# Performance work log

Measured on AMD Instinct MI355X. Metric: run time of the kernel, lower is better.

The kernel has to match this reference:

```python
import jax, jax.numpy as jnp
import numpy as np

BS = 64
DIMS = [1862, 512, 256, 128, 256, 512, 1862]  # layer widths of the generated MLP
W_TOTAL = sum(DIMS[i] * DIMS[i + 1] for i in range(6))   # 2234368
B_TOTAL = sum(DIMS[1:])                                   # 3526


def setup_inputs() -> dict:
    key = jax.random.key(0)
    k1, k2, k3 = jax.random.split(key, 3)
    x = jax.random.normal(k1, (BS, DIMS[0]), dtype=jnp.float32)
    # scale generated weights/biases to keep activations in a sane numeric range
    net_weights = jax.random.normal(k2, (BS, W_TOTAL), dtype=jnp.float32) * 0.02
    net_bias = jax.random.normal(k3, (BS, B_TOTAL), dtype=jnp.float32) * 0.02
    return {"x": x, "net_weights": net_weights, "net_bias": net_bias}


def reference(x, net_weights, net_bias):
    # x: (B, 1862); per-sample weights flattened in net_weights, biases in net_bias.
    h = x
    w_off = 0
    b_off = 0
    for i in range(6):
        din, dout = DIMS[i], DIMS[i + 1]
        W = net_weights[:, w_off:w_off + din * dout].reshape(-1, din, dout)  # (B, din, dout)
        b = net_bias[:, b_off:b_off + dout]                                   # (B, dout)
        h = jnp.einsum('bi,bio->bo', h, W) + b  # batched GEMV + bias
        h = jax.nn.silu(h) if i < 5 else jnp.tanh(h)
        w_off += din * dout
        b_off += dout
    return h[:, None, :]  # (B, 1, 1862), matching torch bmm output shape
```

## Files before the change

kernel.cpp:

```cpp
#include <hip/hip_runtime.h>

#define BS        64
#define W_TOTAL_C 2234368
#define B_TOTAL_C 3526

__device__ __forceinline__ float silu_f(float v) {
    return v / (1.f + __expf(-v));
}

template<int DIN, int DOUT, int KC, int NK, int PNK, int VEC, int BLK,
         bool FINAL, int WOFF, int PBOFF, int FBOFF>
__global__ __launch_bounds__(BLK)
void layer_kernel(const float* __restrict__ hin,
                  const float* __restrict__ wbase,
                  const float* __restrict__ bias,
                  float* __restrict__ outp)
{
    __shared__ float sh[KC];

    const int b   = blockIdx.z;
    const int ky  = blockIdx.y;
    const int k0  = ky * KC;
    const int tid = threadIdx.x;

    for (int i = tid; i < KC; i += BLK) {
        float s;
        if (PNK == 0) {
            s = hin[b * DIN + k0 + i];
        } else {
            s = bias[b * B_TOTAL_C + PBOFF + k0 + i];
            #pragma unroll
            for (int k = 0; k < PNK; ++k)
                s += hin[((size_t)k * BS + b) * DIN + k0 + i];
            s = silu_f(s);
        }
        sh[i] = s;
    }
    __syncthreads();

    const int  o      = (blockIdx.x * BLK + tid) * VEC;
    const bool active = (o < DOUT);

    float a0 = 0.f, a1 = 0.f, a2 = 0.f, a3 = 0.f;
    if (active) {
        const float* wp = wbase + (size_t)b * W_TOTAL_C + WOFF
                                + (size_t)k0 * DOUT + o;
        if (VEC == 4) {
            #pragma unroll 16
            for (int i = 0; i < KC; ++i) {
                const float hv = sh[i];
                const float4 w = *reinterpret_cast<const float4*>(wp);
                a0 = fmaf(hv, w.x, a0);
                a1 = fmaf(hv, w.y, a1);
                a2 = fmaf(hv, w.z, a2);
                a3 = fmaf(hv, w.w, a3);
                wp += DOUT;
            }
        } else {
            #pragma unroll 16
            for (int i = 0; i < KC; ++i) {
                const float hv = sh[i];
                const float2 w = *reinterpret_cast<const float2*>(wp);
                a0 = fmaf(hv, w.x, a0);
                a1 = fmaf(hv, w.y, a1);
                wp += DOUT;
            }
        }
    }

    if (!active) return;

    if (FINAL) {
        float v0 = a0 + bias[b * B_TOTAL_C + FBOFF + o];
        outp[b * DOUT + o] = tanhf(v0);
        if (o + 1 < DOUT) {
            float v1 = a1 + bias[b * B_TOTAL_C + FBOFF + o + 1];
            outp[b * DOUT + o + 1] = tanhf(v1);
        }
    } else {
        float* pp = outp + ((size_t)ky * BS + b) * DOUT + o;
        if (VEC == 4) {
            *reinterpret_cast<float4*>(pp) = make_float4(a0, a1, a2, a3);
        } else {
            pp[0] = a0;
            pp[1] = a1;
        }
    }
}

extern "C" void kernel_launch(void* const* d_in, const int* in_sizes, int n_in,
                              void* d_out, int out_size, void* d_ws, size_t ws_size,
                              hipStream_t stream)
{
    const float* x    = (const float*)d_in[0];
    const float* wts  = (const float*)d_in[1];
    const float* bias = (const float*)d_in[2];
    float* out = (float*)d_out;

    float* p0 = (float*)d_ws;
    float* p1 = p0 + 229376;
    float* p2 = p1 + 65536;
    float* p3 = p2 + 32768;
    float* p4 = p3 + 65536;

    layer_kernel<1862, 512, 266, 7, 0, 4, 128, false,       0,    0,    0>
        <<<dim3(1, 7, BS), 128, 0, stream>>>(x, wts, bias, p0);
    layer_kernel< 512, 256, 128, 4, 7, 2, 128, false,  953344,    0,    0>
        <<<dim3(1, 4, BS), 128, 0, stream>>>(p0, wts, bias, p1);
    layer_kernel< 256, 128,  64, 4, 4, 2,  64, false, 1084416,  512,    0>
        <<<dim3(1, 4, BS),  64, 0, stream>>>(p1, wts, bias, p2);
    layer_kernel< 128, 256,  32, 4, 4, 2, 128, false, 1117184,  768,    0>
        <<<dim3(1, 4, BS), 128, 0, stream>>>(p2, wts, bias, p3);
    layer_kernel< 256, 512,  64, 4, 4, 2, 128, false, 1149952,  896,    0>
        <<<dim3(2, 4, BS), 128, 0, stream>>>(p3, wts, bias, p4);
    layer_kernel< 512, 1862, 512, 1, 4, 2, 256, true, 1281024, 1152, 1664>
        <<<dim3(4, 1, BS), 256, 0, stream>>>(p4, wts, bias, out);
}
```

Baseline: 121.2 us.

## Software-pipeline layers across two batch halves in combined launches

Splits the batch of 64 into two halves of 32 and skews them, so each launch runs layer i for the second half together with layer i+1 for the first half. The goal is to fill the machine in layers that launch too few blocks and to hide launch gaps, at the cost of seven launches instead of six. Layer 0 is also split into 14 K-chunks instead of 7, with a larger partial buffer, and all blocks now use 128 threads. Layer 5 changes from 4 blocks of 256 threads to 8 blocks of 128.

```diff
diff --git a/kernel.cpp b/kernel.cpp
--- a/kernel.cpp
+++ b/kernel.cpp
@@ -1,6 +1,6 @@
 #include <hip/hip_runtime.h>
 
-#define BS        64
+#define BSALL     64
 #define W_TOTAL_C 2234368
 #define B_TOTAL_C 3526
 
@@ -8,85 +8,123 @@
     return v / (1.f + __expf(-v));
 }
 
-template<int DIN, int DOUT, int KC, int NK, int PNK, int VEC, int BLK,
-         bool FINAL, int WOFF, int PBOFF, int FBOFF>
-__global__ __launch_bounds__(BLK)
-void layer_kernel(const float* __restrict__ hin,
-                  const float* __restrict__ wbase,
-                  const float* __restrict__ bias,
-                  float* __restrict__ outp)
+template<int DIN_, int DOUT_, int KC_, int NKY_, int GX_, int PNK_, int VEC_,
+         bool FINAL_, int WOFF_, int PBOFF_, int FBOFF_, int SB_>
+struct LP {
+    static constexpr int  DIN = DIN_, DOUT = DOUT_, KC = KC_, NKY = NKY_,
+                          GX = GX_, PNK = PNK_, VEC = VEC_, WOFF = WOFF_,
+                          PBOFF = PBOFF_, FBOFF = FBOFF_, SB = SB_;
+    static constexpr bool FINAL = FINAL_;
+    static constexpr int  NBLK = GX_ * NKY_ * 32;
+};
+
+template<class P>
+__device__ __forceinline__
+void layer_body(int bid, int tid,
+                const float* __restrict__ hin,
+                float* __restrict__ outp,
+                const float* __restrict__ wbase,
+                const float* __restrict__ bias,
+                float* sh)
 {
-    __shared__ float sh[KC];
+    const int b    = P::SB + (bid & 31);
+    const int rest = bid >> 5;
+    const int ky   = rest % P::NKY;
+    const int gx   = rest / P::NKY;
+    const int k0   = ky * P::KC;
 
-    const int b   = blockIdx.z;
-    const int ky  = blockIdx.y;
-    const int k0  = ky * KC;
-    const int tid = threadIdx.x;
-
-    for (int i = tid; i < KC; i += BLK) {
+    for (int i = tid; i < P::KC; i += 128) {
         float s;
-        if (PNK == 0) {
-            s = hin[b * DIN + k0 + i];
+        if (P::PNK == 0) {
+            s = hin[b * P::DIN + k0 + i];
         } else {
-            s = bias[b * B_TOTAL_C + PBOFF + k0 + i];
+            s = bias[b * B_TOTAL_C + P::PBOFF + k0 + i];
             #pragma unroll
-            for (int k = 0; k < PNK; ++k)
-                s += hin[((size_t)k * BS + b) * DIN + k0 + i];
+            for (int k = 0; k < P::PNK; ++k)
+                s += hin[((size_t)k * BSALL + b) * P::DIN + k0 + i];
             s = silu_f(s);
         }
         sh[i] = s;
     }
     __syncthreads();
 
-    const int  o      = (blockIdx.x * BLK + tid) * VEC;
-    const bool active = (o < DOUT);
+    const int o = (gx * 128 + tid) * P::VEC;
+    if (o >= P::DOUT) return;
 
     float a0 = 0.f, a1 = 0.f, a2 = 0.f, a3 = 0.f;
-    if (active) {
-        const float* wp = wbase + (size_t)b * W_TOTAL_C + WOFF
-                                + (size_t)k0 * DOUT + o;
-        if (VEC == 4) {
-            #pragma unroll 16
-            for (int i = 0; i < KC; ++i) {
-                const float hv = sh[i];
-                const float4 w = *reinterpret_cast<const float4*>(wp);
-                a0 = fmaf(hv, w.x, a0);
-                a1 = fmaf(hv, w.y, a1);
-                a2 = fmaf(hv, w.z, a2);
-                a3 = fmaf(hv, w.w, a3);
-                wp += DOUT;
-            }
-        } else {
-            #pragma unroll 16
-            for (int i = 0; i < KC; ++i) {
-                const float hv = sh[i];
-                const float2 w = *reinterpret_cast<const float2*>(wp);
-                a0 = fmaf(hv, w.x, a0);
-                a1 = fmaf(hv, w.y, a1);
-                wp += DOUT;
-            }
+    const float* wp = wbase + (size_t)b * W_TOTAL_C + P::WOFF
+                            + (size_t)k0 * P::DOUT + o;
+    if (P::VEC == 4) {
+        #pragma unroll 16
+        for (int i = 0; i < P::KC; ++i) {
+            const float hv = sh[i];
+            const float4 w = *reinterpret_cast<const float4*>(wp);
+            a0 = fmaf(hv, w.x, a0);
+            a1 = fmaf(hv, w.y, a1);
+            a2 = fmaf(hv, w.z, a2);
+            a3 = fmaf(hv, w.w, a3);
+            wp += P::DOUT;
+        }
+    } else {
+        #pragma unroll 16
+        for (int i = 0; i < P::KC; ++i) {
+            const float hv = sh[i];
+            const float2 w = *reinterpret_cast<const float2*>(wp);
+            a0 = fmaf(hv, w.x, a0);
+            a1 = fmaf(hv, w.y, a1);
+            wp += P::DOUT;
         }
     }
 
-    if (!active) return;
-
-    if (FINAL) {
-        float v0 = a0 + bias[b * B_TOTAL_C + FBOFF + o];
-        outp[b * DOUT + o] = tanhf(v0);
-        if (o + 1 < DOUT) {
-            float v1 = a1 + bias[b * B_TOTAL_C + FBOFF + o + 1];
-            outp[b * DOUT + o + 1] = tanhf(v1);
+    if (P::FINAL) {
+        float v0 = a0 + bias[b * B_TOTAL_C + P::FBOFF + o];
+        outp[b * P::DOUT + o] = tanhf(v0);
+        if (o + 1 < P::DOUT) {
+            float v1 = a1 + bias[b * B_TOTAL_C + P::FBOFF + o + 1];
+            outp[b * P::DOUT + o + 1] = tanhf(v1);
         }
     } else {
-        float* pp = outp + ((size_t)ky * BS + b) * DOUT + o;
-        if (VEC == 4) {
-            *reinterpret_cast<float4*>(pp) = make_float4(a0, a1, a2, a3);
-        } else {
-            pp[0] = a0;
-            pp[1] = a1;
-        }
+        float* pp = outp + ((size_t)ky * BSALL + b) * P::DOUT + o;
+        if (P::VEC == 4) *reinterpret_cast<float4*>(pp) = make_float4(a0, a1, a2, a3);
+        else { pp[0] = a0; pp[1] = a1; }
     }
 }
+
+template<class A>
+__global__ __launch_bounds__(128)
+void mono_kernel(const float* __restrict__ hinA, float* __restrict__ outA,
+                 const float* __restrict__ wts, const float* __restrict__ bias)
+{
+    __shared__ float sh[512];
+    layer_body<A>(blockIdx.x, threadIdx.x, hinA, outA, wts, bias, sh);
+}
+
+template<class A, class B>
+__global__ __launch_bounds__(128)
+void dual_kernel(const float* __restrict__ hinA, float* __restrict__ outA,
+                 const float* __restrict__ hinB, float* __restrict__ outB,
+                 const float* __restrict__ wts, const float* __restrict__ bias)
+{
+    __shared__ float sh[512];
+    const int bid = blockIdx.x;
+    if (bid < A::NBLK)
+        layer_body<A>(bid, threadIdx.x, hinA, outA, wts, bias, sh);
+    else
+        layer_body<B>(bid - A::NBLK, threadIdx.x, hinB, outB, wts, bias, sh);
+}
+
+using L0A = LP<1862,  512, 133, 14, 1,  0, 4, false,       0,    0,    0,  0>;
+using L0B = LP<1862,  512, 133, 14, 1,  0, 4, false,       0,    0,    0, 32>;
+using L1A = LP< 512,  256, 128,  4, 1, 14, 2, false,  953344,    0,    0,  0>;
+using L1B = LP< 512,  256, 128,  4, 1, 14, 2, false,  953344,    0,    0, 32>;
+using L2A = LP< 256,  128,  64,  4, 1,  4, 2, false, 1084416,  512,    0,  0>;
+using L2B = LP< 256,  128,  64,  4, 1,  4, 2, false, 1084416,  512,    0, 32>;
+using L3A = LP< 128,  256,  32,  4, 1,  4, 2, false, 1117184,  768,    0,  0>;
+using L3B = LP< 128,  256,  32,  4, 1,  4, 2, false, 1117184,  768,    0, 32>;
+using L4A = LP< 256,  512,  64,  4, 2,  4, 2, false, 1149952,  896,    0,  0>;
+using L4B = LP< 256,  512,  64,  4, 2,  4, 2, false, 1149952,  896,    0, 32>;
+using L5A = LP< 512, 1862, 512,  1, 8,  4, 2, true,  1281024, 1152, 1664,  0>;
+using L5B = LP< 512, 1862, 512,  1, 8,  4, 2, true,  1281024, 1152, 1664, 32>;
 
 extern "C" void kernel_launch(void* const* d_in, const int* in_sizes, int n_in,
                               void* d_out, int out_size, void* d_ws, size_t ws_size,
@@ -98,21 +136,21 @@
     float* out = (float*)d_out;
 
     float* p0 = (float*)d_ws;
-    float* p1 = p0 + 229376;
+    float* p1 = p0 + 458752;
     float* p2 = p1 + 65536;
     float* p3 = p2 + 32768;
     float* p4 = p3 + 65536;
 
-    layer_kernel<1862, 512, 266, 7, 0, 4, 128, false,       0,    0,    0>
-        <<<dim3(1, 7, BS), 128, 0, stream>>>(x, wts, bias, p0);
-    layer_kernel< 512, 256, 128, 4, 7, 2, 128, false,  953344,    0,    0>
-        <<<dim3(1, 4, BS), 128, 0, stream>>>(p0, wts, bias, p1);
-    layer_kernel< 256, 128,  64, 4, 4, 2,  64, false, 1084416,  512,    0>
-        <<<dim3(1, 4, BS),  64, 0, stream>>>(p1, wts, bias, p2);
-    layer_kernel< 128, 256,  32, 4, 4, 2, 128, false, 1117184,  768,    0>
-        <<<dim3(1, 4, BS), 128, 0, stream>>>(p2, wts, bias, p3);
-    layer_kernel< 256, 512,  64, 4, 4, 2, 128, false, 1149952,  896,    0>
-        <<<dim3(2, 4, BS), 128, 0, stream>>>(p3, wts, bias, p4);
-    layer_kernel< 512, 1862, 512, 1, 4, 2, 256, true, 1281024, 1152, 1664>
-        <<<dim3(4, 1, BS), 256, 0, stream>>>(p4, wts, bias, out);
+    mono_kernel<L0A><<<dim3(L0A::NBLK), 128, 0, stream>>>(x, p0, wts, bias);
+    dual_kernel<L0B, L1A><<<dim3(L0B::NBLK + L1A::NBLK), 128, 0, stream>>>(
+        x, p0, p0, p1, wts, bias);
+    dual_kernel<L1B, L2A><<<dim3(L1B::NBLK + L2A::NBLK), 128, 0, stream>>>(
+        p0, p1, p1, p2, wts, bias);
+    dual_kernel<L2B, L3A><<<dim3(L2B::NBLK + L3A::NBLK), 128, 0, stream>>>(
+        p1, p2, p2, p3, wts, bias);
+    dual_kernel<L3B, L4A><<<dim3(L3B::NBLK + L4A::NBLK), 128, 0, stream>>>(
+        p2, p3, p3, p4, wts, bias);
+    dual_kernel<L4B, L5A><<<dim3(L4B::NBLK + L5A::NBLK), 128, 0, stream>>>(
+        p3, p4, p4, out, wts, bias);
+    mono_kernel<L5B><<<dim3(L5B::NBLK), 128, 0, stream>>>(p4, out, wts, bias);
 }
```

After: 142.0 us. +17.1%, slower.

## Fuse six layer kernels into one persistent cooperative kernel with grid syncs

Applied to the files above, without the earlier changes.

Replaces six separate layer launches with a single cooperative kernel of 512 blocks that loops over tiles for each layer and uses grid.sync between layers. The goal is to remove per-launch overhead and launch gaps across the memory-bound chain of batched GEMVs. The first layer's K split is also doubled to 14 chunks, which creates more tiles but doubles the partial-sum buffer and the reduction work in layer two. All blocks now use 128 threads, so the final layer runs twice as many smaller tiles, and grid-wide barriers add their own synchronization cost.

```diff
diff --git a/kernel.cpp b/kernel.cpp
--- a/kernel.cpp
+++ b/kernel.cpp
@@ -1,4 +1,7 @@
 #include <hip/hip_runtime.h>
+#include <hip/hip_cooperative_groups.h>
+
+namespace cg = cooperative_groups;
 
 #define BS        64
 #define W_TOTAL_C 2234368
@@ -8,22 +11,23 @@
     return v / (1.f + __expf(-v));
 }
 
-template<int DIN, int DOUT, int KC, int NK, int PNK, int VEC, int BLK,
-         bool FINAL, int WOFF, int PBOFF, int FBOFF>
-__global__ __launch_bounds__(BLK)
-void layer_kernel(const float* __restrict__ hin,
-                  const float* __restrict__ wbase,
-                  const float* __restrict__ bias,
-                  float* __restrict__ outp)
+template<int DIN, int DOUT, int KC, int NKY, int PNK, int VEC, bool FINAL,
+         int WOFF, int PBOFF, int FBOFF>
+__device__ __forceinline__
+void tile_body(int t, int tid,
+               const float* __restrict__ hin,
+               float* __restrict__ outp,
+               const float* __restrict__ wts,
+               const float* __restrict__ bias,
+               float* sh)
 {
-    __shared__ float sh[KC];
+    const int b  = t & 63;
+    const int r  = t >> 6;
+    const int ky = r % NKY;
+    const int gx = r / NKY;
+    const int k0 = ky * KC;
 
-    const int b   = blockIdx.z;
-    const int ky  = blockIdx.y;
-    const int k0  = ky * KC;
-    const int tid = threadIdx.x;
-
-    for (int i = tid; i < KC; i += BLK) {
+    for (int i = tid; i < KC; i += 128) {
         float s;
         if (PNK == 0) {
             s = hin[b * DIN + k0 + i];
@@ -38,13 +42,11 @@
     }
     __syncthreads();
 
-    const int  o      = (blockIdx.x * BLK + tid) * VEC;
-    const bool active = (o < DOUT);
-
-    float a0 = 0.f, a1 = 0.f, a2 = 0.f, a3 = 0.f;
-    if (active) {
-        const float* wp = wbase + (size_t)b * W_TOTAL_C + WOFF
-                                + (size_t)k0 * DOUT + o;
+    const int o = (gx * 128 + tid) * VEC;
+    if (o < DOUT) {
+        float a0 = 0.f, a1 = 0.f, a2 = 0.f, a3 = 0.f;
+        const float* wp = wts + (size_t)b * W_TOTAL_C + WOFF
+                              + (size_t)k0 * DOUT + o;
         if (VEC == 4) {
             #pragma unroll 16
             for (int i = 0; i < KC; ++i) {
@@ -66,26 +68,57 @@
                 wp += DOUT;
             }
         }
-    }
 
-    if (!active) return;
-
-    if (FINAL) {
-        float v0 = a0 + bias[b * B_TOTAL_C + FBOFF + o];
-        outp[b * DOUT + o] = tanhf(v0);
-        if (o + 1 < DOUT) {
-            float v1 = a1 + bias[b * B_TOTAL_C + FBOFF + o + 1];
-            outp[b * DOUT + o + 1] = tanhf(v1);
-        }
-    } else {
-        float* pp = outp + ((size_t)ky * BS + b) * DOUT + o;
-        if (VEC == 4) {
-            *reinterpret_cast<float4*>(pp) = make_float4(a0, a1, a2, a3);
+        if (FINAL) {
+            float v0 = a0 + bias[b * B_TOTAL_C + FBOFF + o];
+            outp[b * DOUT + o] = tanhf(v0);
+            if (o + 1 < DOUT) {
+                float v1 = a1 + bias[b * B_TOTAL_C + FBOFF + o + 1];
+                outp[b * DOUT + o + 1] = tanhf(v1);
+            }
         } else {
-            pp[0] = a0;
-            pp[1] = a1;
+            float* pp = outp + ((size_t)ky * BS + b) * DOUT + o;
+            if (VEC == 4) *reinterpret_cast<float4*>(pp) = make_float4(a0, a1, a2, a3);
+            else { pp[0] = a0; pp[1] = a1; }
         }
     }
+    __syncthreads();
+}
+
+__global__ __launch_bounds__(128)
+void meta_coop(const float* __restrict__ x,
+               const float* __restrict__ wts,
+               const float* __restrict__ bias,
+               float* __restrict__ out,
+               float* p0, float* p1, float* p2, float* p3, float* p4)
+{
+    cg::grid_group grid = cg::this_grid();
+    __shared__ float sh[512];
+    const int tid = threadIdx.x;
+
+    for (int t = blockIdx.x; t < 14 * 64; t += gridDim.x)
+        tile_body<1862,  512, 133, 14,  0, 4, false,       0,    0,    0>(
+            t, tid, x, p0, wts, bias, sh);
+    grid.sync();
+    for (int t = blockIdx.x; t < 4 * 64; t += gridDim.x)
+        tile_body< 512,  256, 128,  4, 14, 2, false,  953344,    0,    0>(
+            t, tid, p0, p1, wts, bias, sh);
+    grid.sync();
+    for (int t = blockIdx.x; t < 4 * 64; t += gridDim.x)
+        tile_body< 256,  128,  64,  4,  4, 2, false, 1084416,  512,    0>(
+            t, tid, p1, p2, wts, bias, sh);
+    grid.sync();
+    for (int t = blockIdx.x; t < 4 * 64; t += gridDim.x)
+        tile_body< 128,  256,  32,  4,  4, 2, false, 1117184,  768,    0>(
+            t, tid, p2, p3, wts, bias, sh);
+    grid.sync();
+    for (int t = blockIdx.x; t < 8 * 64; t += gridDim.x)
+        tile_body< 256,  512,  64,  4,  4, 2, false, 1149952,  896,    0>(
+            t, tid, p3, p4, wts, bias, sh);
+    grid.sync();
+    for (int t = blockIdx.x; t < 8 * 64; t += gridDim.x)
+        tile_body< 512, 1862, 512,  1,  4, 2, true,  1281024, 1152, 1664>(
+            t, tid, p4, out, wts, bias, sh);
 }
 
 extern "C" void kernel_launch(void* const* d_in, const int* in_sizes, int n_in,
@@ -98,21 +131,13 @@
     float* out = (float*)d_out;
 
     float* p0 = (float*)d_ws;
-    float* p1 = p0 + 229376;
+    float* p1 = p0 + 458752;
     float* p2 = p1 + 65536;
     float* p3 = p2 + 32768;
     float* p4 = p3 + 65536;
 
-    layer_kernel<1862, 512, 266, 7, 0, 4, 128, false,       0,    0,    0>
-        <<<dim3(1, 7, BS), 128, 0, stream>>>(x, wts, bias, p0);
-    layer_kernel< 512, 256, 128, 4, 7, 2, 128, false,  953344,    0,    0>
-        <<<dim3(1, 4, BS), 128, 0, stream>>>(p0, wts, bias, p1);
-    layer_kernel< 256, 128,  64, 4, 4, 2,  64, false, 1084416,  512,    0>
-        <<<dim3(1, 4, BS),  64, 0, stream>>>(p1, wts, bias, p2);
-    layer_kernel< 128, 256,  32, 4, 4, 2, 128, false, 1117184,  768,    0>
-        <<<dim3(1, 4, BS), 128, 0, stream>>>(p2, wts, bias, p3);
-    layer_kernel< 256, 512,  64, 4, 4, 2, 128, false, 1149952,  896,    0>
-        <<<dim3(2, 4, BS), 128, 0, stream>>>(p3, wts, bias, p4);
-    layer_kernel< 512, 1862, 512, 1, 4, 2, 256, true, 1281024, 1152, 1664>
-        <<<dim3(4, 1, BS), 256, 0, stream>>>(p4, wts, bias, out);
+    void* args[] = { (void*)&x, (void*)&wts, (void*)&bias, (void*)&out,
+                     (void*)&p0, (void*)&p1, (void*)&p2, (void*)&p3, (void*)&p4 };
+    hipLaunchCooperativeKernel((const void*)meta_coop,
+                               dim3(512), dim3(128), args, 0, stream);
 }
```

New measurement: 408.8 us. 237% more time.
